# Kernel tuning notes

Measured on AMD Instinct MI355X. Metric: run time of the kernel, lower is better.

## Reference

```python
import jax, jax.numpy as jnp
import numpy as np

N_NODES = 20000


def _gcn_norm(edge_index, num_nodes):
    """PyG GCNConv normalization: add self-loops, symmetric deg^-1/2 norm."""
    src, dst = edge_index[0], edge_index[1]
    loop = jnp.arange(num_nodes, dtype=src.dtype)
    src = jnp.concatenate([src, loop])
    dst = jnp.concatenate([dst, loop])
    deg = jax.ops.segment_sum(jnp.ones_like(dst, dtype=jnp.float32), dst,
                              num_segments=num_nodes)
    dis = jnp.where(deg > 0, jax.lax.rsqrt(deg), 0.0)
    norm = dis[src] * dis[dst]  # [E+N]
    return src, dst, norm


def _gcn_layer(h, W, b, src, dst, norm, num_nodes):
    h = h @ W                                  # [N, out]
    msg = h[src] * norm[:, None]               # gather + scale  [E+N, out]
    out = jax.ops.segment_sum(msg, dst, num_segments=num_nodes)
    return out + b


def setup_inputs() -> dict:
    key = jax.random.key(0)
    ks = jax.random.split(key, 8)
    E = 320000
    x = jax.random.normal(ks[0], (N_NODES, 256), dtype=jnp.float32)
    W1 = jax.random.normal(ks[1], (256, 256), dtype=jnp.float32) * (1.0 / np.sqrt(256))
    b1 = jnp.zeros((256,), dtype=jnp.float32)
    W2 = jax.random.normal(ks[2], (256, 128), dtype=jnp.float32) * (1.0 / np.sqrt(256))
    b2 = jnp.zeros((128,), dtype=jnp.float32)
    W3 = jax.random.normal(ks[3], (128, 64), dtype=jnp.float32) * (1.0 / np.sqrt(128))
    b3 = jnp.zeros((64,), dtype=jnp.float32)
    edge_index = jax.random.randint(ks[4], (2, E), 0, N_NODES, dtype=jnp.int64)
    return {"x": x, "W1": W1, "b1": b1, "W2": W2, "b2": b2,
            "W3": W3, "b3": b3, "edge_index": edge_index}


def reference(x, W1, b1, W2, b2, W3, b3, edge_index):
    n = x.shape[0]
    src, dst, norm = _gcn_norm(edge_index, n)
    h = jax.nn.relu(_gcn_layer(x, W1, b1, src, dst, norm, n))
    h = jax.nn.relu(_gcn_layer(h, W2, b2, src, dst, norm, n))
    return _gcn_layer(h, W3, b3, src, dst, norm, n)
```

## Files before the change

kernel.cpp:

```cpp
#include <hip/hip_runtime.h>


typedef _Float16 half8_t __attribute__((ext_vector_type(8)));
typedef float floatx16 __attribute__((ext_vector_type(16)));

#define ELLW 96

__device__ __forceinline__ int detect_is64_block(const void* ei) {
    __shared__ int s_is64;
    const int t = threadIdx.x;
    if (t == 0) s_is64 = 1;
    __syncthreads();
    if (t < 64) {
        const int* q = (const int*)ei;
        if (q[2 * t + 1] != 0) s_is64 = 0;
    }
    __syncthreads();
    return s_is64;
}

__global__ __launch_bounds__(256) void init_kernel(
        int* __restrict__ cnt, const float* __restrict__ W1,
        _Float16* __restrict__ Wt1, int N) {
    const int id = blockIdx.x * 256 + threadIdx.x;
    {
        int n = id >> 8, k = id & 255;
        Wt1[n * 256 + k] = (_Float16)W1[k * 256 + n];
    }
    if (id < N) cnt[id] = 0;
}

__device__ void fill_ell_body(int blk, const void* ei, int* __restrict__ cnt,
                              int* __restrict__ ell, int E) {
    int is64 = detect_is64_block(ei);
    int e0 = (blk * 256 + threadIdx.x) * 2;
    int s0 = 0, s1 = 0, d0 = 0, d1 = 0, n = 0;
    if (is64) {
        const long long* src = (const long long*)ei;
        const long long* dst = src + E;
        if (e0 + 1 < E) {
            int4 vs = *(const int4*)(src + e0);
            int4 vd = *(const int4*)(dst + e0);
            s0 = vs.x; s1 = vs.z; d0 = vd.x; d1 = vd.z; n = 2;
        } else if (e0 < E) { s0 = (int)src[e0]; d0 = (int)dst[e0]; n = 1; }
    } else {
        const int* src = (const int*)ei;
        const int* dst = src + E;
        if (e0 + 1 < E) {
            int2 vs = *(const int2*)(src + e0);
            int2 vd = *(const int2*)(dst + e0);
            s0 = vs.x; s1 = vs.y; d0 = vd.x; d1 = vd.y; n = 2;
        } else if (e0 < E) { s0 = src[e0]; d0 = dst[e0]; n = 1; }
    }
    if (n >= 1) {
        int slot = atomicAdd(&cnt[d0], 1);
        if (slot < ELLW) ell[d0 * ELLW + slot] = s0;
    }
    if (n == 2) {
        int slot = atomicAdd(&cnt[d1], 1);
        if (slot < ELLW) ell[d1 * ELLW + slot] = s1;
    }
}

__device__ void wconv23_body(int blk, const float* __restrict__ W2,
                             const float* __restrict__ W3,
                             _Float16* __restrict__ Wt2, _Float16* __restrict__ Wt3) {
    int id = blk * 256 + threadIdx.x;
    if (id < 32768) {
        int n = id >> 8, k = id & 255;
        Wt2[n * 256 + k] = (_Float16)W2[k * 128 + n];
    } else if (id < 40960) {
        int i = id - 32768;
        int n = i >> 7, k = i & 127;
        Wt3[n * 128 + k] = (_Float16)W3[k * 64 + n];
    }
}

template <typename AT, bool SCALE>
__device__ void gemm_body(int bx, int by, const AT* __restrict__ A,
                          const _Float16* __restrict__ Wt, const int* __restrict__ cnt,
                          _Float16* __restrict__ C, int M, int N, int K) {
    constexpr int BM = 128, BN = 64, BK = 64, PAD = 8;
    __shared__ _Float16 As[BM][BK + PAD];
    __shared__ _Float16 Bs[BN][BK + PAD];
    __shared__ float disS[BM];
    const int tid = threadIdx.x;
    const int wave = tid >> 6, lane = tid & 63;
    const int row0 = bx * BM, col0 = by * BN;

    if constexpr (SCALE) {
        if (tid < BM) {
            int r = row0 + tid;
            disS[tid] = (r < M) ? rsqrtf((float)(cnt[r] + 1)) : 0.f;
        }
    }

    const int ar0 = tid >> 2, ar1 = ar0 + 64;
    const int ac  = (tid & 3) * 16;
    const int br  = tid >> 2;
    const int bc  = (tid & 3) * 16;
    const long long arow0 = (long long)(row0 + ar0) * K;
    const long long arow1 = (long long)(row0 + ar1) * K;
    const long long brow  = (long long)(col0 + br) * K;
    const bool a0ok = (row0 + ar0) < M, a1ok = (row0 + ar1) < M;
    const float4 f4z = make_float4(0.f, 0.f, 0.f, 0.f);

    float4 pa0[4] = {f4z, f4z, f4z, f4z};
    float4 pa1[4] = {f4z, f4z, f4z, f4z};
    float4 pb0, pb1;

    auto loadAB = [&](int k0) {
        if constexpr (sizeof(AT) == 2) {
            const _Float16* p0 = (const _Float16*)A + arow0 + k0 + ac;
            const _Float16* p1 = (const _Float16*)A + arow1 + k0 + ac;
            if (a0ok) { pa0[0] = *(const float4*)p0; pa0[1] = *(const float4*)(p0 + 8); }
            if (a1ok) { pa1[0] = *(const float4*)p1; pa1[1] = *(const float4*)(p1 + 8); }
        } else {
            const float* p0 = (const float*)A + arow0 + k0 + ac;
            const float* p1 = (const float*)A + arow1 + k0 + ac;
            if (a0ok) {
                #pragma unroll
                for (int j = 0; j < 4; ++j) pa0[j] = *(const float4*)(p0 + 4 * j);
            }
            if (a1ok) {
                #pragma unroll
                for (int j = 0; j < 4; ++j) pa1[j] = *(const float4*)(p1 + 4 * j);
            }
        }
        pb0 = *(const float4*)(Wt + brow + k0 + bc);
        pb1 = *(const float4*)(Wt + brow + k0 + bc + 8);
    };
    auto storeAB = [&]() {
        if constexpr (sizeof(AT) == 2) {
            *(float4*)&As[ar0][ac]     = pa0[0];
            *(float4*)&As[ar0][ac + 8] = pa0[1];
            *(float4*)&As[ar1][ac]     = pa1[0];
            *(float4*)&As[ar1][ac + 8] = pa1[1];
        } else {
            half8_t h;
            const float* f0 = (const float*)pa0;
            #pragma unroll
            for (int j = 0; j < 8; ++j) h[j] = (_Float16)f0[j];
            *(half8_t*)&As[ar0][ac] = h;
            #pragma unroll
            for (int j = 0; j < 8; ++j) h[j] = (_Float16)f0[8 + j];
            *(half8_t*)&As[ar0][ac + 8] = h;
            const float* f1 = (const float*)pa1;
            #pragma unroll
            for (int j = 0; j < 8; ++j) h[j] = (_Float16)f1[j];
            *(half8_t*)&As[ar1][ac] = h;
            #pragma unroll
            for (int j = 0; j < 8; ++j) h[j] = (_Float16)f1[8 + j];
            *(half8_t*)&As[ar1][ac + 8] = h;
        }
        *(float4*)&Bs[br][bc]     = pb0;
        *(float4*)&Bs[br][bc + 8] = pb1;
    };

    loadAB(0);
    storeAB();
    __syncthreads();

    floatx16 acc0, acc1;
    #pragma unroll
    for (int i = 0; i < 16; ++i) { acc0[i] = 0.f; acc1[i] = 0.f; }

    const _Float16* ap  = &As[wave * 32 + (lane & 31)][(lane >> 5) * 8];
    const _Float16* bp0 = &Bs[lane & 31][(lane >> 5) * 8];
    const _Float16* bp1 = &Bs[32 + (lane & 31)][(lane >> 5) * 8];

    const int niter = K / BK;
    for (int it = 0; it < niter; ++it) {
        const bool more = (it + 1) < niter;
        if (more) loadAB((it + 1) * BK);
        #pragma unroll
        for (int s = 0; s < 4; ++s) {
            half8_t a  = *(const half8_t*)(ap  + s * 16);
            half8_t b0 = *(const half8_t*)(bp0 + s * 16);
            half8_t b1 = *(const half8_t*)(bp1 + s * 16);
            acc0 = __builtin_amdgcn_mfma_f32_32x32x16_f16(a, b0, acc0, 0, 0, 0);
            acc1 = __builtin_amdgcn_mfma_f32_32x32x16_f16(a, b1, acc1, 0, 0, 0);
        }
        if (more) {
            __syncthreads();
            storeAB();
            __syncthreads();
        }
    }

    const int colb = lane & 31, q = lane >> 5;
    #pragma unroll
    for (int r = 0; r < 16; ++r) {
        int rl = wave * 32 + (r & 3) + 8 * (r >> 2) + 4 * q;
        int row = row0 + rl;
        if (row >= M) continue;
        float d = SCALE ? disS[rl] : 1.0f;
        C[(long long)row * N + col0 + colb]      = (_Float16)(acc0[r] * d);
        C[(long long)row * N + col0 + 32 + colb] = (_Float16)(acc1[r] * d);
    }
}

__global__ __launch_bounds__(256) void fused_build_kernel(
        const float* x, const _Float16* Wt1, _Float16* C, int M, int gM, int nGemm,
        const void* ei, int* cnt, int* ell, int E, int nFill,
        const float* W2, const float* W3, _Float16* Wt2, _Float16* Wt3) {
    const int b = blockIdx.x;
    if (b < nGemm) {
        gemm_body<float, false>(b % gM, b / gM, x, Wt1, nullptr, C, M, 256, 256);
    } else if (b < nGemm + nFill) {
        fill_ell_body(b - nGemm, ei, cnt, ell, E);
    } else {
        wconv23_body(b - nGemm - nFill, W2, W3, Wt2, Wt3);
    }
}

__global__ __launch_bounds__(256) void gemm_kernel(
        const _Float16* A, const _Float16* Wt, const int* cnt, _Float16* C,
        int M, int N, int K) {
    gemm_body<_Float16, true>(blockIdx.x, blockIdx.y, A, Wt, cnt, C, M, N, K);
}

__device__ __forceinline__ void vload8h(float* d, const _Float16* p) {
    half8_t v = *(const half8_t*)p;
    #pragma unroll
    for (int i = 0; i < 8; ++i) d[i] = (float)v[i];
}

template <int F, bool OUT_HALF, int U, bool SCALE_SRC>
__global__ __launch_bounds__(256) void agg_kernel(
        const _Float16* __restrict__ hs, const int* __restrict__ cnt,
        const float* __restrict__ bias, const int* __restrict__ ell,
        void* __restrict__ outv, int N, int do_relu) {
    constexpr int LPE = F / 8;
    constexpr int EPL = 64 / LPE;
    constexpr int STEP = U * EPL;
    const int wave = threadIdx.x >> 6;
    const int lane = threadIdx.x & 63;
    const int n = blockIdx.x * 4 + wave;
    if (n >= N) return;
    const int fl = lane % LPE;
    const int es = lane / LPE;
    const int fo = fl * 8;
    const int deg = cnt[n];
    const float dn = rsqrtf((float)(deg + 1));

    float acc[8];
    if (es == 0) {
        vload8h(acc, hs + (long long)n * F + fo);
        if constexpr (SCALE_SRC) {
            #pragma unroll
            for (int k = 0; k < 8; ++k) acc[k] *= dn;
        }
    } else {
        #pragma unroll
        for (int v = 0; v < 8; ++v) acc[v] = 0.f;
    }

    const int g  = deg < ELLW ? deg : ELLW;
    const int s0 = n * ELLW, s1 = s0 + g;
    int j = s0;
    for (; j + STEP <= s1; j += STEP) {
        int idx[U];
        #pragma unroll
        for (int u = 0; u < U; ++u) idx[u] = ell[j + u * EPL + es];
        float ds[U];
        if constexpr (SCALE_SRC) {
            #pragma unroll
            for (int u = 0; u < U; ++u)
                ds[u] = rsqrtf((float)(cnt[idx[u]] + 1));
        }
        float v[U][8];
        #pragma unroll
        for (int u = 0; u < U; ++u)
            vload8h(v[u], hs + (long long)idx[u] * F + fo);
        #pragma unroll
        for (int u = 0; u < U; ++u) {
            #pragma unroll
            for (int k = 0; k < 8; ++k)
                acc[k] += SCALE_SRC ? v[u][k] * ds[u] : v[u][k];
        }
    }
    if (j < s1) {
        #pragma unroll
        for (int u = 0; u < U; ++u) {
            int e = j + u * EPL + es;
            if (e < s1) {
                int ii = ell[e];
                float sc = SCALE_SRC ? rsqrtf((float)(cnt[ii] + 1)) : 1.0f;
                float v[8];
                vload8h(v, hs + (long long)ii * F + fo);
                #pragma unroll
                for (int k = 0; k < 8; ++k) acc[k] += v[k] * sc;
            }
        }
    }

    #pragma unroll
    for (int offd = 32; offd >= LPE; offd >>= 1) {
        #pragma unroll
        for (int k = 0; k < 8; ++k) acc[k] += __shfl_down(acc[k], offd);
    }

    if (lane < LPE) {
        float4 b0 = *(const float4*)(bias + fo);
        float4 b1 = *(const float4*)(bias + fo + 4);
        float bb[8] = {b0.x, b0.y, b0.z, b0.w, b1.x, b1.y, b1.z, b1.w};
        float o[8];
        #pragma unroll
        for (int k = 0; k < 8; ++k) {
            float val = dn * acc[k] + bb[k];
            o[k] = do_relu ? fmaxf(val, 0.f) : val;
        }
        if constexpr (OUT_HALF) {
            half8_t h;
            #pragma unroll
            for (int k = 0; k < 8; ++k) h[k] = (_Float16)o[k];
            *(half8_t*)((_Float16*)outv + (long long)n * F + fo) = h;
        } else {
            float* op = (float*)outv + (long long)n * F + fo;
            *(float4*)op       = make_float4(o[0], o[1], o[2], o[3]);
            *(float4*)(op + 4) = make_float4(o[4], o[5], o[6], o[7]);
        }
    }
}

extern "C" void kernel_launch(void* const* d_in, const int* in_sizes, int n_in,
                              void* d_out, int out_size, void* d_ws, size_t ws_size,
                              hipStream_t stream) {
    const float* x  = (const float*)d_in[0];
    const float* W1 = (const float*)d_in[1];
    const float* b1 = (const float*)d_in[2];
    const float* W2 = (const float*)d_in[3];
    const float* b2 = (const float*)d_in[4];
    const float* W3 = (const float*)d_in[5];
    const float* b3 = (const float*)d_in[6];
    const void*  ei = d_in[7];

    const int N = in_sizes[0] / 256;
    const int E = in_sizes[7] / 2;

    size_t cur = 0;
    auto alloc = [&](size_t bytes) -> void* {
        void* p = (char*)d_ws + cur;
        cur += (bytes + 255) & ~(size_t)255;
        return p;
    };
    int*      cnt  = (int*)alloc((size_t)N * 4);
    int*      ell  = (int*)alloc((size_t)N * ELLW * 4);
    _Float16* Wt1  = (_Float16*)alloc(256 * 256 * 2);
    _Float16* Wt2  = (_Float16*)alloc(128 * 256 * 2);
    _Float16* Wt3  = (_Float16*)alloc(64 * 128 * 2);
    _Float16* bufC = (_Float16*)alloc((size_t)N * 256 * 2);
    _Float16* bufH = (_Float16*)alloc((size_t)N * 256 * 2);
    (void)ws_size; (void)n_in; (void)out_size;

    const int gM    = (N + 127) / 128;
    const int nGm1  = gM * 4;
    const int nFill = (E / 2 + 255) / 256;
    const int nWcv  = (40960 + 255) / 256;
    const int gAgg  = (N + 3) / 4;

    init_kernel<<<256, 256, 0, stream>>>(cnt, W1, Wt1, N);
    fused_build_kernel<<<nGm1 + nFill + nWcv, 256, 0, stream>>>(
        x, Wt1, bufC, N, gM, nGm1, ei, cnt, ell, E, nFill, W2, W3, Wt2, Wt3);

    agg_kernel<256, true, 4, true><<<gAgg, 256, 0, stream>>>(
        bufC, cnt, b1, ell, bufH, N, 1);
    gemm_kernel<<<dim3(gM, 2), 256, 0, stream>>>(bufH, Wt2, cnt, bufC, N, 128, 256);
    agg_kernel<128, true, 4, false><<<gAgg, 256, 0, stream>>>(
        bufC, cnt, b2, ell, bufH, N, 1);
    gemm_kernel<<<dim3(gM, 1), 256, 0, stream>>>(bufH, Wt3, cnt, bufC, N, 64, 128);
    agg_kernel<64, false, 2, false><<<gAgg, 256, 0, stream>>>(
        bufC, cnt, b3, ell, d_out, N, 0);
}
```

Before: 165.1 us.

## Pre-convert x to fp16 in init kernel and simplify build kernel

The fp32 x matrix is converted to fp16 in a separate pass inside the init kernel, which now also transposes and converts W1, W2 and W3. The first GEMM then reads fp16 input instead of converting fp32 tiles on the fly, which shrinks its register footprint. Edge filling now uses one edge per thread with scalar loads instead of two per thread. The cost is an extra full read and write of x through global memory before the first GEMM, and finer-grained fill blocks.

```diff
diff --git a/kernel.cpp b/kernel.cpp
--- a/kernel.cpp
+++ b/kernel.cpp
@@ -20,64 +20,63 @@
 }
 
 __global__ __launch_bounds__(256) void init_kernel(
-        int* __restrict__ cnt, const float* __restrict__ W1,
-        _Float16* __restrict__ Wt1, int N) {
-    const int id = blockIdx.x * 256 + threadIdx.x;
-    {
+        const float* __restrict__ x, _Float16* __restrict__ xh,
+        const float* __restrict__ W1, const float* __restrict__ W2,
+        const float* __restrict__ W3, _Float16* __restrict__ Wt1,
+        _Float16* __restrict__ Wt2, _Float16* __restrict__ Wt3,
+        int* __restrict__ cnt, int N, int nXh) {
+    const int b = blockIdx.x;
+    if (b < nXh) {
+        const long long i = ((long long)b * 256 + threadIdx.x) * 8;
+        if (i < (long long)N * 256) {
+            float4 v0 = *(const float4*)(x + i);
+            float4 v1 = *(const float4*)(x + i + 4);
+            half8_t h;
+            h[0] = (_Float16)v0.x; h[1] = (_Float16)v0.y;
+            h[2] = (_Float16)v0.z; h[3] = (_Float16)v0.w;
+            h[4] = (_Float16)v1.x; h[5] = (_Float16)v1.y;
+            h[6] = (_Float16)v1.z; h[7] = (_Float16)v1.w;
+            *(half8_t*)(xh + i) = h;
+        }
+        return;
+    }
+    const int id = (b - nXh) * 256 + threadIdx.x;
+    if (id < N) cnt[id] = 0;
+    if (id < 65536) {
         int n = id >> 8, k = id & 255;
         Wt1[n * 256 + k] = (_Float16)W1[k * 256 + n];
-    }
-    if (id < N) cnt[id] = 0;
+    } else if (id < 98304) {
+        int i = id - 65536;
+        int n = i >> 8, k = i & 255;
+        Wt2[n * 256 + k] = (_Float16)W2[k * 128 + n];
+    } else if (id < 106496) {
+        int i = id - 98304;
+        int n = i >> 7, k = i & 127;
+        Wt3[n * 128 + k] = (_Float16)W3[k * 64 + n];
+    }
 }
 
 __device__ void fill_ell_body(int blk, const void* ei, int* __restrict__ cnt,
                               int* __restrict__ ell, int E) {
     int is64 = detect_is64_block(ei);
-    int e0 = (blk * 256 + threadIdx.x) * 2;
-    int s0 = 0, s1 = 0, d0 = 0, d1 = 0, n = 0;
+    int e = blk * 256 + threadIdx.x;
+    if (e >= E) return;
+    int s, d;
     if (is64) {
         const long long* src = (const long long*)ei;
-        const long long* dst = src + E;
-        if (e0 + 1 < E) {
-            int4 vs = *(const int4*)(src + e0);
-            int4 vd = *(const int4*)(dst + e0);
-            s0 = vs.x; s1 = vs.z; d0 = vd.x; d1 = vd.z; n = 2;
-        } else if (e0 < E) { s0 = (int)src[e0]; d0 = (int)dst[e0]; n = 1; }
+        s = (int)src[e];
+        d = (int)src[E + e];
     } else {
         const int* src = (const int*)ei;
-        const int* dst = src + E;
-        if (e0 + 1 < E) {
-            int2 vs = *(const int2*)(src + e0);
-            int2 vd = *(const int2*)(dst + e0);
-            s0 = vs.x; s1 = vs.y; d0 = vd.x; d1 = vd.y; n = 2;
-        } else if (e0 < E) { s0 = src[e0]; d0 = dst[e0]; n = 1; }
-    }
-    if (n >= 1) {
-        int slot = atomicAdd(&cnt[d0], 1);
-        if (slot < ELLW) ell[d0 * ELLW + slot] = s0;
-    }
-    if (n == 2) {
-        int slot = atomicAdd(&cnt[d1], 1);
-        if (slot < ELLW) ell[d1 * ELLW + slot] = s1;
-    }
-}
-
-__device__ void wconv23_body(int blk, const float* __restrict__ W2,
-                             const float* __restrict__ W3,
-                             _Float16* __restrict__ Wt2, _Float16* __restrict__ Wt3) {
-    int id = blk * 256 + threadIdx.x;
-    if (id < 32768) {
-        int n = id >> 8, k = id & 255;
-        Wt2[n * 256 + k] = (_Float16)W2[k * 128 + n];
-    } else if (id < 40960) {
-        int i = id - 32768;
-        int n = i >> 7, k = i & 127;
-        Wt3[n * 128 + k] = (_Float16)W3[k * 64 + n];
-    }
-}
-
-template <typename AT, bool SCALE>
-__device__ void gemm_body(int bx, int by, const AT* __restrict__ A,
+        s = src[e];
+        d = src[E + e];
+    }
+    int slot = atomicAdd(&cnt[d], 1);
+    if (slot < ELLW) ell[d * ELLW + slot] = s;
+}
+
+template <bool SCALE>
+__device__ void gemm_body(int bx, int by, const _Float16* __restrict__ A,
                           const _Float16* __restrict__ Wt, const int* __restrict__ cnt,
                           _Float16* __restrict__ C, int M, int N, int K) {
     constexpr int BM = 128, BN = 64, BK = 64, PAD = 8;
@@ -105,56 +104,23 @@
     const bool a0ok = (row0 + ar0) < M, a1ok = (row0 + ar1) < M;
     const float4 f4z = make_float4(0.f, 0.f, 0.f, 0.f);
 
-    float4 pa0[4] = {f4z, f4z, f4z, f4z};
-    float4 pa1[4] = {f4z, f4z, f4z, f4z};
-    float4 pb0, pb1;
+    float4 pa00 = f4z, pa01 = f4z, pa10 = f4z, pa11 = f4z, pb0, pb1;
 
     auto loadAB = [&](int k0) {
-        if constexpr (sizeof(AT) == 2) {
-            const _Float16* p0 = (const _Float16*)A + arow0 + k0 + ac;
-            const _Float16* p1 = (const _Float16*)A + arow1 + k0 + ac;
-            if (a0ok) { pa0[0] = *(const float4*)p0; pa0[1] = *(const float4*)(p0 + 8); }
-            if (a1ok) { pa1[0] = *(const float4*)p1; pa1[1] = *(const float4*)(p1 + 8); }
-        } else {
-            const float* p0 = (const float*)A + arow0 + k0 + ac;
-            const float* p1 = (const float*)A + arow1 + k0 + ac;
-            if (a0ok) {
-                #pragma unroll
-                for (int j = 0; j < 4; ++j) pa0[j] = *(const float4*)(p0 + 4 * j);
-            }
-            if (a1ok) {
-                #pragma unroll
-                for (int j = 0; j < 4; ++j) pa1[j] = *(const float4*)(p1 + 4 * j);
-            }
-        }
+        const _Float16* p0 = A + arow0 + k0 + ac;
+        const _Float16* p1 = A + arow1 + k0 + ac;
+        if (a0ok) { pa00 = *(const float4*)p0; pa01 = *(const float4*)(p0 + 8); }
+        if (a1ok) { pa10 = *(const float4*)p1; pa11 = *(const float4*)(p1 + 8); }
         pb0 = *(const float4*)(Wt + brow + k0 + bc);
         pb1 = *(const float4*)(Wt + brow + k0 + bc + 8);
     };
     auto storeAB = [&]() {
-        if constexpr (sizeof(AT) == 2) {
-            *(float4*)&As[ar0][ac]     = pa0[0];
-            *(float4*)&As[ar0][ac + 8] = pa0[1];
-            *(float4*)&As[ar1][ac]     = pa1[0];
-            *(float4*)&As[ar1][ac + 8] = pa1[1];
-        } else {
-            half8_t h;
-            const float* f0 = (const float*)pa0;
-            #pragma unroll
-            for (int j = 0; j < 8; ++j) h[j] = (_Float16)f0[j];
-            *(half8_t*)&As[ar0][ac] = h;
-            #pragma unroll
-            for (int j = 0; j < 8; ++j) h[j] = (_Float16)f0[8 + j];
-            *(half8_t*)&As[ar0][ac + 8] = h;
-            const float* f1 = (const float*)pa1;
-            #pragma unroll
-            for (int j = 0; j < 8; ++j) h[j] = (_Float16)f1[j];
-            *(half8_t*)&As[ar1][ac] = h;
-            #pragma unroll
-            for (int j = 0; j < 8; ++j) h[j] = (_Float16)f1[8 + j];
-            *(half8_t*)&As[ar1][ac + 8] = h;
-        }
-        *(float4*)&Bs[br][bc]     = pb0;
-        *(float4*)&Bs[br][bc + 8] = pb1;
+        *(float4*)&As[ar0][ac]     = pa00;
+        *(float4*)&As[ar0][ac + 8] = pa01;
+        *(float4*)&As[ar1][ac]     = pa10;
+        *(float4*)&As[ar1][ac + 8] = pa11;
+        *(float4*)&Bs[br][bc]      = pb0;
+        *(float4*)&Bs[br][bc + 8]  = pb1;
     };
 
     loadAB(0);
@@ -201,23 +167,20 @@
 }
 
 __global__ __launch_bounds__(256) void fused_build_kernel(
-        const float* x, const _Float16* Wt1, _Float16* C, int M, int gM, int nGemm,
-        const void* ei, int* cnt, int* ell, int E, int nFill,
-        const float* W2, const float* W3, _Float16* Wt2, _Float16* Wt3) {
+        const _Float16* xh, const _Float16* Wt1, _Float16* C, int M, int gM,
+        int nGemm, const void* ei, int* cnt, int* ell, int E) {
     const int b = blockIdx.x;
     if (b < nGemm) {
-        gemm_body<float, false>(b % gM, b / gM, x, Wt1, nullptr, C, M, 256, 256);
-    } else if (b < nGemm + nFill) {
+        gemm_body<false>(b % gM, b / gM, xh, Wt1, nullptr, C, M, 256, 256);
+    } else {
         fill_ell_body(b - nGemm, ei, cnt, ell, E);
-    } else {
-        wconv23_body(b - nGemm - nFill, W2, W3, Wt2, Wt3);
     }
 }
 
 __global__ __launch_bounds__(256) void gemm_kernel(
         const _Float16* A, const _Float16* Wt, const int* cnt, _Float16* C,
         int M, int N, int K) {
-    gemm_body<_Float16, true>(blockIdx.x, blockIdx.y, A, Wt, cnt, C, M, N, K);
+    gemm_body<true>(blockIdx.x, blockIdx.y, A, Wt, cnt, C, M, N, K);
 }
 
 __device__ __forceinline__ void vload8h(float* d, const _Float16* p) {
@@ -354,15 +317,19 @@
     _Float16* bufH = (_Float16*)alloc((size_t)N * 256 * 2);
     (void)ws_size; (void)n_in; (void)out_size;
 
+    _Float16* xh = bufH;
+
     const int gM    = (N + 127) / 128;
     const int nGm1  = gM * 4;
-    const int nFill = (E / 2 + 255) / 256;
-    const int nWcv  = (40960 + 255) / 256;
+    const int nFill = (E + 255) / 256;
+    const int nXh   = (N * 256 / 8 + 255) / 256;
+    const int nWc   = 416;
     const int gAgg  = (N + 3) / 4;
 
-    init_kernel<<<256, 256, 0, stream>>>(cnt, W1, Wt1, N);
-    fused_build_kernel<<<nGm1 + nFill + nWcv, 256, 0, stream>>>(
-        x, Wt1, bufC, N, gM, nGm1, ei, cnt, ell, E, nFill, W2, W3, Wt2, Wt3);
+    init_kernel<<<nXh + nWc, 256, 0, stream>>>(
+        x, xh, W1, W2, W3, Wt1, Wt2, Wt3, cnt, N, nXh);
+    fused_build_kernel<<<nGm1 + nFill, 256, 0, stream>>>(
+        xh, Wt1, bufC, N, gM, nGm1, ei, cnt, ell, E);
 
     agg_kernel<256, true, 4, true><<<gAgg, 256, 0, stream>>>(
         bufC, cnt, b1, ell, bufH, N, 1);
```

Measured after the change: 167.8 us (median of 2 runs). About the same (+1.6%).
